# Optimization experiments

Measured on AMD Instinct MI355X. Metric: run time of the kernel, lower is better.

The kernel has to match this reference:

```python
import jax, jax.numpy as jnp
import numpy as np

B, N, H, E, P = 2, 20000, 128, 200000, 3


def _mlp2(x, w1, b1, w2, b2):
    # Linear -> SiLU -> Linear
    return jax.nn.silu(x @ w1 + b1) @ w2 + b2


def setup_inputs() -> dict:
    key = jax.random.key(0)
    ks = iter(jax.random.split(key, 40))
    def nrm(shape, s=0.05):
        return jax.random.normal(next(ks), shape, dtype=jnp.float32) * s
    inp = {
        "features": jax.random.normal(next(ks), (B, N, H), dtype=jnp.float32),
        "positions": jax.random.normal(next(ks), (B, N, P), dtype=jnp.float32),
        "edge_index_up": jax.random.randint(next(ks), (2, E), 0, N, dtype=jnp.int32),
        "edge_index_down": jax.random.randint(next(ks), (2, E), 0, N, dtype=jnp.int32),
        "degree_up": jax.random.uniform(next(ks), (N,), minval=1.0, maxval=32.0, dtype=jnp.float32),
        "degree_down": jax.random.uniform(next(ks), (N,), minval=1.0, maxval=32.0, dtype=jnp.float32),
    }
    for name in ("up", "down"):
        inp[f"w_msg1_{name}"] = nrm((2 * H + 1, H)); inp[f"b_msg1_{name}"] = jnp.zeros((H,), jnp.float32)
        inp[f"w_msg2_{name}"] = nrm((H, H));         inp[f"b_msg2_{name}"] = jnp.zeros((H,), jnp.float32)
        inp[f"w_pos1_{name}"] = nrm((H, H));         inp[f"b_pos1_{name}"] = jnp.zeros((H,), jnp.float32)
        inp[f"w_pos2_{name}"] = nrm((H, 1));         inp[f"b_pos2_{name}"] = jnp.zeros((1,), jnp.float32)
    inp["w_upd1"] = nrm((2 * H, H)); inp["b_upd1"] = jnp.zeros((H,), jnp.float32)
    inp["w_upd2"] = nrm((H, H));     inp["b_upd2"] = jnp.zeros((H,), jnp.float32)
    return inp


def reference(features, positions, edge_index_up, edge_index_down, degree_up, degree_down,
              w_msg1_up, b_msg1_up, w_msg2_up, b_msg2_up,
              w_pos1_up, b_pos1_up, w_pos2_up, b_pos2_up,
              w_msg1_down, b_msg1_down, w_msg2_down, b_msg2_down,
              w_pos1_down, b_pos1_down, w_pos2_down, b_pos2_down,
              w_upd1, b_upd1, w_upd2, b_upd2):
    n_neighborhoods = 2
    msg_acc = jnp.zeros_like(features)
    pos_upd = jnp.zeros_like(positions)
    neighborhoods = [
        (edge_index_up, degree_up,
         (w_msg1_up, b_msg1_up, w_msg2_up, b_msg2_up),
         (w_pos1_up, b_pos1_up, w_pos2_up, b_pos2_up)),
        (edge_index_down, degree_down,
         (w_msg1_down, b_msg1_down, w_msg2_down, b_msg2_down),
         (w_pos1_down, b_pos1_down, w_pos2_down, b_pos2_down)),
    ]
    for edge_index, degree, msg_p, pos_p in neighborhoods:
        src, dst = edge_index[0], edge_index[1]
        h_src = features[:, src, :]                     # [B, E, H] gather
        h_dst = features[:, dst, :]                     # [B, E, H] gather
        rel_pos = positions[:, src, :] - positions[:, dst, :]  # [B, E, P]
        dist = jnp.linalg.norm(rel_pos, axis=-1, keepdims=True)  # [B, E, 1]
        msg_input = jnp.concatenate([h_src, h_dst, dist], axis=-1)  # [B, E, 2H+1]
        messages = _mlp2(msg_input, *msg_p)             # [B, E, H]
        agg = jnp.zeros_like(features).at[:, dst, :].add(messages)  # scatter-add over dim 1
        agg = agg / jnp.clip(degree, 1.0, None)[None, :, None]
        msg_acc = msg_acc + agg
        weights = jnp.tanh(_mlp2(messages, *pos_p))     # [B, E, 1]
        pos_upd = pos_upd + jnp.zeros_like(positions).at[:, dst, :].add(weights * rel_pos)
    feat_update = _mlp2(jnp.concatenate([features, msg_acc], axis=-1), w_upd1, b_upd1, w_upd2, b_upd2)
    updated_features = features + feat_update
    updated_positions = positions + pos_upd / n_neighborhoods
    return updated_features, updated_positions
```

## Files before the change

### kernel.cpp

```cpp
#include <hip/hip_runtime.h>

#define BB 2
#define NN 20000
#define HH 128
#define EE 200000
#define TR 96
#define NEB 2084
#define NBLK 79

typedef unsigned short u16;
typedef __attribute__((ext_vector_type(4))) float f32x4;
typedef __bf16 bf16x8 __attribute__((ext_vector_type(8)));

#define MFMA(a, b, c) __builtin_amdgcn_mfma_f32_16x16x32_bf16((a), (b), (c), 0, 0, 0)

__device__ __forceinline__ float bf2f(u16 u) {
    union { unsigned int i; float f; } v; v.i = ((unsigned int)u) << 16; return v.f;
}
__device__ __forceinline__ u16 f2bf(float f) {
    union { __bf16 h; u16 u; } v; v.h = (__bf16)f; return v.u;
}
#if __has_builtin(__builtin_amdgcn_rcpf)
__device__ __forceinline__ float rcpf(float x) { return __builtin_amdgcn_rcpf(x); }
#else
__device__ __forceinline__ float rcpf(float x) { return 1.f / x; }
#endif
__device__ __forceinline__ float silu_f(float z) { return z * rcpf(1.f + __expf(-z)); }
__device__ __forceinline__ float ldv(const void* p, long i, int f) {
    return f ? ((const float*)p)[i] : bf2f(((const u16*)p)[i]);
}

__global__ __launch_bounds__(256) void detect_zero_kernel(const u16* __restrict__ f,
                                                          int* __restrict__ flag,
                                                          int* __restrict__ cnt) {
    int i = blockIdx.x * 256 + threadIdx.x;
    if (i < 40000) cnt[i] = 0;
    if (blockIdx.x == 0) {
        int tid = threadIdx.x;
        u16 v = f[tid * 2];
        int e = (v >> 7) & 0xFF;
        int ok = (e >= 101 && e <= 143) ? 1 : 0;
        __shared__ int c;
        if (tid == 0) c = 0;
        __syncthreads();
        atomicAdd(&c, ok);
        __syncthreads();
        if (tid == 0) *flag = (c < 200) ? 1 : 0;
    }
}

#define C5TOT 5281540
#define FTOT 180224
#define R0 5240000
#define R1 (R0 + C5TOT)
#define R2 (R1 + FTOT)
#define R3 (R2 + 2 * EE)
struct P18 { const void* p[18]; };
struct P8 { const void* w[8]; };

__global__ __launch_bounds__(256) void setup_kernel(
    P18 cp, P8 wf, const int* __restrict__ eu, const int* __restrict__ ed,
    float* __restrict__ ws_acc, u16* __restrict__ canon, u16* __restrict__ fbase,
    int* __restrict__ cnt_up, int* __restrict__ cnt_dn, const int* __restrict__ flag)
{
    long i = (long)blockIdx.x * 256 + threadIdx.x;
    if (i < R0) { ws_acc[i] = 0.f; return; }
    if (i < R1) {
        static const int off[19] = {
            0, 5120000, 5240000, 5260000, 5280000,
            5280128, 5280256, 5280384, 5280512, 5280640,
            5280642, 5280770, 5280898, 5281026, 5281154, 5281282,
            5281284, 5281412, 5281540 };
        static const int rsz[18] = {
            5120000, 120000, 20000, 20000,
            128, 128, 128, 128, 128, 1,
            128, 128, 128, 128, 128, 1,
            128, 128 };
        static const int soff[18] = {
            0, 0, 0, 0,
            32768, 0, 0, 0, 0, 0,
            32768, 0, 0, 0, 0, 0,
            0, 0 };
        int j = (int)(i - R0);
        int isf = *flag;
        int t = 0;
#pragma unroll 1
        while (j >= off[t + 1]) ++t;
        int k = j - off[t];
        u16 v = 0;
        if (k < rsz[t]) v = f2bf(ldv(cp.p[t], (long)soff[t] + k, isf));
        canon[j] = v;
        return;
    }
    if (i < R2) {
        static const int foff[9] = { 0, 32768, 49152, 65536, 98304, 114688,
                                     131072, 163840, 180224 };
        int j = (int)(i - R1);
        int isf = *flag;
        int t = 0;
#pragma unroll 1
        while (j >= foff[t + 1]) ++t;
        int m = j - foff[t];
        int jj = m & 7, lane = (m >> 3) & 63, nt = (m >> 9) & 7, kt = m >> 12;
        int k = kt * 32 + ((lane >> 4) * 8) + jj;
        int n = nt * 16 + (lane & 15);
        fbase[j] = f2bf(ldv(wf.w[t], (long)k * 128 + n, isf));
        return;
    }
    if (i < R3) {
        int e = (int)(i - R2);
        if (e < EE) atomicAdd(&cnt_up[eu[EE + e]], 1);
        else atomicAdd(&cnt_dn[ed[EE + e - EE]], 1);
    }
}

__global__ __launch_bounds__(256) void gemm_fuse_kernel(
    const void* __restrict__ w2u, const void* __restrict__ p1u,
    const void* __restrict__ b2u, const void* __restrict__ bp1u,
    const void* __restrict__ w2d, const void* __restrict__ p1d,
    const void* __restrict__ b2d, const void* __restrict__ bp1d,
    u16* __restrict__ fragu, u16* __restrict__ fragd,
    u16* __restrict__ cbp1u, u16* __restrict__ cbp1d,
    const int* __restrict__ flag)
{
    const int dir = blockIdx.x >> 6;
    const int idx = (blockIdx.x & 63) * 256 + threadIdx.x;
    const int k = idx >> 7, n = idx & 127;
    const int isf = *flag;
    const void* W2 = dir ? w2d : w2u;
    const void* P1 = dir ? p1d : p1u;
    float s = 0.f;
#pragma unroll 4
    for (int m = 0; m < 128; ++m)
        s += ldv(W2, (long)k * 128 + m, isf) * ldv(P1, (long)m * 128 + n, isf);
    u16* dst = dir ? fragd : fragu;
    dst[(((k >> 5) * 8 + (n >> 4)) * 64 + ((k >> 3) & 3) * 16 + (n & 15)) * 8 + (k & 7)] = f2bf(s);
    if (idx < 128) {
        const void* B2 = dir ? b2d : b2u;
        const void* BP1 = dir ? bp1d : bp1u;
        float t = 0.f;
#pragma unroll 4
        for (int m = 0; m < 128; ++m)
            t += ldv(B2, m, isf) * ldv(P1, (long)m * 128 + idx, isf);
        (dir ? cbp1d : cbp1u)[idx] = f2bf(t + ldv(BP1, idx, isf));
    }
}

struct SP { const int* cnt[2]; int* cur[2]; int* bsum[2]; };

__global__ __launch_bounds__(256) void scan1_kernel(SP p) {
    int half = blockIdx.x / NBLK;
    int b = blockIdx.x - half * NBLK;
    int t = threadIdx.x;
    int i = b * 256 + t;
    __shared__ int buf[256];
    int v = (i < NN) ? p.cnt[half][i] : 0;
    buf[t] = v;
    __syncthreads();
    for (int s = 1; s < 256; s <<= 1) {
        int x = (t >= s) ? buf[t - s] : 0;
        __syncthreads();
        buf[t] += x;
        __syncthreads();
    }
    if (i < NN) p.cur[half][i] = buf[t] - v;
    if (t == 255) p.bsum[half][b] = buf[255];
}

__global__ __launch_bounds__(256) void scan2_kernel(int* __restrict__ bu, int* __restrict__ bd) {
    __shared__ int buf[2][128];
    int half = threadIdx.x >> 7, t = threadIdx.x & 127;
    int* bs = half ? bd : bu;
    int v = (t < NBLK) ? bs[t] : 0;
    buf[half][t] = v;
    __syncthreads();
    for (int s = 1; s < 128; s <<= 1) {
        int x = (t >= s) ? buf[half][t - s] : 0;
        __syncthreads();
        buf[half][t] += x;
        __syncthreads();
    }
    if (t < NBLK) bs[t] = buf[half][t] - v;
}

__global__ void scatter2_kernel(const int* __restrict__ eu, const int* __restrict__ ed,
                                int* __restrict__ cu, const int* __restrict__ bu,
                                int* __restrict__ cd, const int* __restrict__ bd,
                                int* __restrict__ su, int* __restrict__ sd) {
    int e = blockIdx.x * 256 + threadIdx.x;
    if (e < EE) {
        int d = eu[EE + e];
        int p = atomicAdd(&cu[d], 1) + bu[d >> 8];
        su[p] = e;
    } else {
        e -= EE;
        if (e < EE) {
            int d = ed[EE + e];
            int p = atomicAdd(&cd[d], 1) + bd[d >> 8];
            sd[p] = e;
        }
    }
}

struct EP {
    const int* eidx; const int* es; const u16* deg;
    const u16* fW1; const u16* fW2; const u16* fP1;
    const u16* w1last; const u16* bias1; const u16* bias2;
    const u16* biasp1; const u16* wp2; const u16* biasp2;
};

__global__ __launch_bounds__(512, 4) void edge_kernel(
    const u16* __restrict__ feat, const u16* __restrict__ posit,
    EP up, EP dn,
    float* __restrict__ msg_base, float* __restrict__ pos_base)
{
    const int tid = threadIdx.x;
    const int lane = tid & 63;
    const int wv = tid >> 6;
    const int half = blockIdx.x / (BB * NEB);
    const int rem = blockIdx.x - half * (BB * NEB);
    const int bb = rem / NEB;
    const int s0 = (rem - bb * NEB) * TR;
    const EP P = half ? dn : up;
    float* msg_acc = msg_base + (size_t)bb * NN * HH;
    float* pos_acc = pos_base + (size_t)bb * NN * 3;

    __shared__ u16 sA[TR][136];
    __shared__ u16 sB[TR][136];
    __shared__ u16 sC[TR][136];
    __shared__ float sInv[TR];
    __shared__ int sDst[TR];

    {
        const int r = tid >> 2, part = tid & 3;
        if (r < TR) {
            int slot = s0 + r; if (slot >= EE) slot = EE - 1;
            int e = P.es[slot];
            int s = P.eidx[e];
            int d = P.eidx[EE + e];
            if (part == 0) {
                sDst[r] = d;
                sInv[r] = 1.f / fmaxf(bf2f(P.deg[d]), 1.f);
                const u16* ps = posit + ((size_t)bb * NN + s) * 3;
                const u16* pd = posit + ((size_t)bb * NN + d) * 3;
                float dx = bf2f(ps[0]) - bf2f(pd[0]);
                float dy = bf2f(ps[1]) - bf2f(pd[1]);
                float dz = bf2f(ps[2]) - bf2f(pd[2]);
                *(float4*)&sC[r][128] =
                    make_float4(sqrtf(dx * dx + dy * dy + dz * dz), dx, dy, dz);
            }
            const uint4* fs = (const uint4*)(feat + ((size_t)bb * NN + s) * HH);
            const uint4* fd = (const uint4*)(feat + ((size_t)bb * NN + d) * HH);
            uint4* as = (uint4*)&sA[r][part * 32];
            uint4* ad = (uint4*)&sB[r][part * 32];
#pragma unroll
            for (int i = 0; i < 4; ++i) { as[i] = fs[part * 4 + i]; ad[i] = fd[part * 4 + i]; }
        }
    }
    __syncthreads();

    const int wm = wv >> 2;
    const int wn = wv & 3;
    const int rbase = wm * 48;
    const int mrow = lane & 15;
    const int kq = (lane >> 4) * 8;
    const int crow = (lane >> 4) * 4;
    const int ccol = lane & 15;

    f32x4 acc[3][2];
#pragma unroll
    for (int mt = 0; mt < 3; ++mt) {
        acc[mt][0] = (f32x4){0.f, 0.f, 0.f, 0.f};
        acc[mt][1] = (f32x4){0.f, 0.f, 0.f, 0.f};
    }
#pragma unroll
    for (int kt = 0; kt < 8; ++kt) {
        const u16* Xb = (kt < 4) ? &sA[0][0] : &sB[0][0];
        const int kk = (kt & 3) * 32 + kq;
        bf16x8 bw0 = *(const bf16x8*)(P.fW1 + (size_t)(((kt * 8 + wn * 2) * 64 + lane) * 8));
        bf16x8 bw1 = *(const bf16x8*)(P.fW1 + (size_t)(((kt * 8 + wn * 2 + 1) * 64 + lane) * 8));
#pragma unroll
        for (int mt = 0; mt < 3; ++mt) {
            bf16x8 a = *(const bf16x8*)(Xb + (rbase + mt * 16 + mrow) * 136 + kk);
            acc[mt][0] = MFMA(a, bw0, acc[mt][0]);
            acc[mt][1] = MFMA(a, bw1, acc[mt][1]);
        }
    }

#pragma unroll
    for (int n2 = 0; n2 < 2; ++n2) {
        const int col = (wn * 2 + n2) * 16 + ccol;
        const float wl = bf2f(P.w1last[col]);
        const float bb1 = bf2f(P.bias1[col]);
#pragma unroll
        for (int mt = 0; mt < 3; ++mt) {
#pragma unroll
            for (int r = 0; r < 4; ++r) {
                const int row = rbase + mt * 16 + crow + r;
                const float dist = ((const float*)&sC[row][128])[0];
                float z = fmaf(dist, wl, acc[mt][n2][r]) + bb1;
                sC[row][col] = f2bf(silu_f(z));
            }
        }
    }
    __syncthreads();

    f32x4 facc[3][4];
#pragma unroll
    for (int mt = 0; mt < 3; ++mt)
#pragma unroll
        for (int j = 0; j < 4; ++j) facc[mt][j] = (f32x4){0.f, 0.f, 0.f, 0.f};
    const int nt0 = wn * 4;
#pragma unroll
    for (int kt = 0; kt < 4; ++kt) {
        const int kk = kt * 32 + kq;
        bf16x8 bw[4];
#pragma unroll
        for (int j = 0; j < 4; ++j) {
            const int nt = nt0 + j;
            const size_t off = (nt & 8)
                ? (size_t)(16384 + ((kt * 8 + (nt & 7)) * 64 + lane) * 8)
                : (size_t)(((kt * 8 + nt) * 64 + lane) * 8);
            bw[j] = *(const bf16x8*)(P.fW2 + off);
        }
#pragma unroll
        for (int mt = 0; mt < 3; ++mt) {
            bf16x8 a = *(const bf16x8*)(&sC[0][0] + (rbase + mt * 16 + mrow) * 136 + kk);
#pragma unroll
            for (int j = 0; j < 4; ++j) facc[mt][j] = MFMA(a, bw[j], facc[mt][j]);
        }
    }

    if (wn < 2) {
#pragma unroll
        for (int j = 0; j < 4; ++j) {
            const int col = (nt0 + j) * 16 + ccol;
            const float b2v = bf2f(P.bias2[col]);
#pragma unroll
            for (int mt = 0; mt < 3; ++mt) {
#pragma unroll
                for (int r = 0; r < 4; ++r) {
                    const int row = rbase + mt * 16 + crow + r;
                    sA[row][col] = f2bf(facc[mt][j][r] + b2v);
                }
            }
        }
    } else {
#pragma unroll
        for (int j = 0; j < 4; ++j) {
            const int col = (nt0 - 8 + j) * 16 + ccol;
            const float fbv = bf2f(P.biasp1[col]);
#pragma unroll
            for (int mt = 0; mt < 3; ++mt) {
#pragma unroll
                for (int r = 0; r < 4; ++r) {
                    const int row = rbase + mt * 16 + crow + r;
                    sB[row][col] = f2bf(silu_f(facc[mt][j][r] + fbv));
                }
            }
        }
    }
    __syncthreads();

    {
        const int scol = tid & 127;
        const int r0 = (tid >> 7) * 24;
        float vals[24];
#pragma unroll
        for (int j = 0; j < 24; ++j) vals[j] = bf2f(sA[r0 + j][scol]);
        float accv = 0.f;
        int dprev = sDst[r0];
        float invprev = sInv[r0];
#pragma unroll
        for (int j = 0; j < 24; ++j) {
            const int r = r0 + j;
            int dcur = sDst[r];
            if (dcur != dprev) {
                unsafeAtomicAdd(&msg_acc[(size_t)dprev * HH + scol], accv * invprev);
                accv = 0.f; dprev = dcur; invprev = sInv[r];
            }
            accv += (s0 + r < EE) ? vals[j] : 0.f;
        }
        unsafeAtomicAdd(&msg_acc[(size_t)dprev * HH + scol], accv * invprev);
    }

    {
        const int r = tid >> 2, q = tid & 3;
        if (r < TR) {
            const unsigned* t32 = (const unsigned*)&sB[r][q * 32];
            const unsigned* w32 = (const unsigned*)(P.wp2 + q * 32);
            float p = 0.f;
#pragma unroll
            for (int k = 0; k < 16; ++k) {
                unsigned a = t32[k], b = w32[k];
                union { unsigned i; float f; } al, ah, bl, bh;
                al.i = a << 16; ah.i = a & 0xffff0000u;
                bl.i = b << 16; bh.i = b & 0xffff0000u;
                p = fmaf(al.f, bl.f, p);
                p = fmaf(ah.f, bh.f, p);
            }
            p += __shfl_xor(p, 1);
            p += __shfl_xor(p, 2);
            if (q == 0 && s0 + r < EE) {
                float wgt = tanhf(p + bf2f(P.biasp2[0]));
                const float* rp = (const float*)&sC[r][128];
                const size_t pb = (size_t)sDst[r] * 3;
                unsafeAtomicAdd(&pos_acc[pb + 0], wgt * rp[1]);
                unsafeAtomicAdd(&pos_acc[pb + 1], wgt * rp[2]);
                unsafeAtomicAdd(&pos_acc[pb + 2], wgt * rp[3]);
            }
        }
    }
}

__global__ __launch_bounds__(256) void update_kernel(
    const void* __restrict__ rawfeat, const void* __restrict__ rawpos,
    const u16* __restrict__ fU1, const u16* __restrict__ bu1,
    const u16* __restrict__ fU2, const u16* __restrict__ bu2,
    void* __restrict__ outp, const float* __restrict__ magg, const float* __restrict__ pacc,
    const int* __restrict__ flag)
{
    const int tid = threadIdx.x;
    const int lane = tid & 63;
    const int wv = tid >> 6;
    const int row0 = blockIdx.x * 64;
    const int isf = *flag;

    __shared__ u16 sA[64][136];
    __shared__ u16 sB[64][136];

    if (isf) {
        const float* fp = (const float*)rawfeat + (size_t)row0 * HH;
        for (int i = tid; i < 1024; i += 256) {
            int r = i >> 4, c = (i & 15) * 8;
            float4 v0 = *(const float4*)(fp + (size_t)r * HH + c);
            float4 v1 = *(const float4*)(fp + (size_t)r * HH + c + 4);
            uint4 o;
            o.x = (unsigned)f2bf(v0.x) | ((unsigned)f2bf(v0.y) << 16);
            o.y = (unsigned)f2bf(v0.z) | ((unsigned)f2bf(v0.w) << 16);
            o.z = (unsigned)f2bf(v1.x) | ((unsigned)f2bf(v1.y) << 16);
            o.w = (unsigned)f2bf(v1.z) | ((unsigned)f2bf(v1.w) << 16);
            *(uint4*)&sA[r][c] = o;
        }
    } else {
        const uint4* fp = (const uint4*)((const u16*)rawfeat + (size_t)row0 * HH);
        for (int i = tid; i < 1024; i += 256) {
            int r = i >> 4, c = i & 15;
            *(uint4*)&sA[r][c * 8] = fp[i];
        }
    }
    {
        const float4* am = (const float4*)(magg) + (size_t)row0 * 32;
        for (int i = tid; i < 2048; i += 256) {
            int r = i >> 5;
            float4 v = am[i];
            int c = (i & 31) * 4;
            sB[r][c + 0] = f2bf(v.x);
            sB[r][c + 1] = f2bf(v.y);
            sB[r][c + 2] = f2bf(v.z);
            sB[r][c + 3] = f2bf(v.w);
        }
    }
    __syncthreads();

    const int nt0 = wv * 2;
    const int mrow = lane & 15;
    const int kq = (lane >> 4) * 8;
    const int crow = (lane >> 4) * 4;
    const int ccol = lane & 15;

    f32x4 acc[4][2];
#pragma unroll
    for (int mt = 0; mt < 4; ++mt) {
        acc[mt][0] = (f32x4){0.f, 0.f, 0.f, 0.f};
        acc[mt][1] = (f32x4){0.f, 0.f, 0.f, 0.f};
    }
#pragma unroll
    for (int kt = 0; kt < 8; ++kt) {
        const u16* Xb = (kt < 4) ? &sA[0][0] : &sB[0][0];
        const int kk = (kt & 3) * 32 + kq;
        bf16x8 bw0 = *(const bf16x8*)(fU1 + (size_t)(((kt * 8 + nt0) * 64 + lane) * 8));
        bf16x8 bw1 = *(const bf16x8*)(fU1 + (size_t)(((kt * 8 + nt0 + 1) * 64 + lane) * 8));
#pragma unroll
        for (int mt = 0; mt < 4; ++mt) {
            bf16x8 a = *(const bf16x8*)(Xb + (mt * 16 + mrow) * 136 + kk);
            acc[mt][0] = MFMA(a, bw0, acc[mt][0]);
            acc[mt][1] = MFMA(a, bw1, acc[mt][1]);
        }
    }
    __syncthreads();

#pragma unroll
    for (int mt = 0; mt < 4; ++mt) {
#pragma unroll
        for (int n2 = 0; n2 < 2; ++n2) {
            const int col = (nt0 + n2) * 16 + ccol;
            const float bb = bf2f(bu1[col]);
#pragma unroll
            for (int r = 0; r < 4; ++r) {
                const int row = mt * 16 + crow + r;
                sB[row][col] = f2bf(silu_f(acc[mt][n2][r] + bb));
            }
        }
    }
    __syncthreads();

#pragma unroll
    for (int mt = 0; mt < 4; ++mt) {
        acc[mt][0] = (f32x4){0.f, 0.f, 0.f, 0.f};
        acc[mt][1] = (f32x4){0.f, 0.f, 0.f, 0.f};
    }
#pragma unroll
    for (int kt = 0; kt < 4; ++kt) {
        const int kk = kt * 32 + kq;
        bf16x8 bw0 = *(const bf16x8*)(fU2 + (size_t)(((kt * 8 + nt0) * 64 + lane) * 8));
        bf16x8 bw1 = *(const bf16x8*)(fU2 + (size_t)(((kt * 8 + nt0 + 1) * 64 + lane) * 8));
#pragma unroll
        for (int mt = 0; mt < 4; ++mt) {
            bf16x8 a = *(const bf16x8*)(&sB[0][0] + (mt * 16 + mrow) * 136 + kk);
            acc[mt][0] = MFMA(a, bw0, acc[mt][0]);
            acc[mt][1] = MFMA(a, bw1, acc[mt][1]);
        }
    }
#pragma unroll
    for (int mt = 0; mt < 4; ++mt) {
#pragma unroll
        for (int n2 = 0; n2 < 2; ++n2) {
            const int col = (nt0 + n2) * 16 + ccol;
            const float bb = bf2f(bu2[col]);
#pragma unroll
            for (int r = 0; r < 4; ++r) {
                const int row = mt * 16 + crow + r;
                const size_t idx = (size_t)(row0 + row) * HH + col;
                if (isf) {
                    float base = ((const float*)rawfeat)[idx];
                    ((float*)outp)[idx] = acc[mt][n2][r] + bb + base;
                } else {
                    float base = bf2f(sA[row][col]);
                    ((u16*)outp)[idx] = f2bf(acc[mt][n2][r] + bb + base);
                }
            }
        }
    }

    if (tid < 192) {
        int i = row0 * 3 + tid;
        float x = pacc[i];
        if (isf) {
            float base = ((const float*)rawpos)[i];
            ((float*)outp)[5120000 + i] = base + 0.5f * x;
        } else {
            float base = bf2f(((const u16*)rawpos)[i]);
            ((u16*)outp)[5120000 + i] = f2bf(base + 0.5f * x);
        }
    }
}

extern "C" void kernel_launch(void* const* d_in, const int* in_sizes, int n_in,
                              void* d_out, int out_size, void* d_ws, size_t ws_size,
                              hipStream_t stream)
{
    float* ws_msg  = (float*)d_ws;
    float* ws_pos  = (float*)((char*)d_ws + 20480000);
    int*   cnt_up  = (int*)((char*)d_ws + 20960000);
    int*   cnt_dn  = (int*)((char*)d_ws + 21040000);
    int*   cur_up  = (int*)((char*)d_ws + 21120000);
    int*   cur_dn  = (int*)((char*)d_ws + 21200000);
    int*   bsum_up = (int*)((char*)d_ws + 21280000);
    int*   bsum_dn = (int*)((char*)d_ws + 21280400);
    int*   es_up   = (int*)((char*)d_ws + 21280800);
    int*   es_dn   = (int*)((char*)d_ws + 22080800);
    u16*   fbase   = (u16*)((char*)d_ws + 22880800);
    u16*   canon   = (u16*)((char*)d_ws + 23241248);
    int*   flag    = (int*)((char*)d_ws + 33804328);
    if (ws_size < 33804332ULL) return;

    u16* f_m1u = fbase;
    u16* f_m2u = fbase + 32768;
    u16* f_p1u = fbase + 49152;
    u16* f_m1d = fbase + 65536;
    u16* f_m2d = fbase + 98304;
    u16* f_p1d = fbase + 114688;
    u16* f_u1  = fbase + 131072;
    u16* f_u2  = fbase + 163840;

    u16* cfeat  = canon;
    u16* cpos   = canon + 5120000;
    u16* cdgu   = canon + 5240000;
    u16* cdgd   = canon + 5260000;
    u16* cw1lu  = canon + 5280000;
    u16* cb1u   = canon + 5280128;
    u16* cb2u   = canon + 5280256;
    u16* cbp1u  = canon + 5280384;
    u16* cwp2u  = canon + 5280512;
    u16* cbp2u  = canon + 5280640;
    u16* cw1ld  = canon + 5280642;
    u16* cb1d   = canon + 5280770;
    u16* cb2d   = canon + 5280898;
    u16* cbp1d  = canon + 5281026;
    u16* cwp2d  = canon + 5281154;
    u16* cbp2d  = canon + 5281282;
    u16* cbu1   = canon + 5281284;
    u16* cbu2   = canon + 5281412;

    const int* ei_up = (const int*)d_in[2];
    const int* ei_dn = (const int*)d_in[3];

    detect_zero_kernel<<<157, 256, 0, stream>>>((const u16*)d_in[0], flag, cnt_up);

    P18 cp;
    cp.p[0] = d_in[0];  cp.p[1] = d_in[1];  cp.p[2] = d_in[4];  cp.p[3] = d_in[5];
    cp.p[4] = d_in[6];  cp.p[5] = d_in[7];  cp.p[6] = d_in[9];  cp.p[7] = d_in[11];
    cp.p[8] = d_in[12]; cp.p[9] = d_in[13];
    cp.p[10] = d_in[14]; cp.p[11] = d_in[15]; cp.p[12] = d_in[17]; cp.p[13] = d_in[19];
    cp.p[14] = d_in[20]; cp.p[15] = d_in[21];
    cp.p[16] = d_in[23]; cp.p[17] = d_in[25];
    P8 wsf;
    wsf.w[0] = d_in[6];  wsf.w[1] = d_in[8];  wsf.w[2] = d_in[10]; wsf.w[3] = d_in[14];
    wsf.w[4] = d_in[16]; wsf.w[5] = d_in[18]; wsf.w[6] = d_in[22]; wsf.w[7] = d_in[24];
    setup_kernel<<<(R3 + 255) / 256, 256, 0, stream>>>(cp, wsf, ei_up, ei_dn,
                                                       ws_msg, canon, fbase,
                                                       cnt_up, cnt_dn, flag);

    gemm_fuse_kernel<<<128, 256, 0, stream>>>(d_in[8], d_in[10], d_in[9], d_in[11],
                                              d_in[16], d_in[18], d_in[17], d_in[19],
                                              f_p1u, f_p1d, cbp1u, cbp1d, flag);

    SP sp;
    sp.cnt[0] = cnt_up; sp.cnt[1] = cnt_dn;
    sp.cur[0] = cur_up; sp.cur[1] = cur_dn;
    sp.bsum[0] = bsum_up; sp.bsum[1] = bsum_dn;
    scan1_kernel<<<2 * NBLK, 256, 0, stream>>>(sp);
    scan2_kernel<<<1, 256, 0, stream>>>(bsum_up, bsum_dn);
    scatter2_kernel<<<(2 * EE + 255) / 256, 256, 0, stream>>>(ei_up, ei_dn, cur_up, bsum_up,
                                                              cur_dn, bsum_dn, es_up, es_dn);

    EP up, dn;
    up.eidx = ei_up; up.es = es_up; up.deg = cdgu;
    up.fW1 = f_m1u; up.fW2 = f_m2u; up.fP1 = f_p1u;
    up.w1last = cw1lu; up.bias1 = cb1u; up.bias2 = cb2u;
    up.biasp1 = cbp1u; up.wp2 = cwp2u; up.biasp2 = cbp2u;
    dn.eidx = ei_dn; dn.es = es_dn; dn.deg = cdgd;
    dn.fW1 = f_m1d; dn.fW2 = f_m2d; dn.fP1 = f_p1d;
    dn.w1last = cw1ld; dn.bias1 = cb1d; dn.bias2 = cb2d;
    dn.biasp1 = cbp1d; dn.wp2 = cwp2d; dn.biasp2 = cbp2d;
    edge_kernel<<<2 * BB * NEB, 512, 0, stream>>>(cfeat, cpos, up, dn, ws_msg, ws_pos);

    update_kernel<<<625, 256, 0, stream>>>(d_in[0], d_in[1], f_u1, cbu1, f_u2, cbu2,
                                           d_out, ws_msg, ws_pos, flag);
}
```

Measured before the change: 537.1 us.

## Remap edge workgroups across XCDs and run-length merge position atomics

Workgroup IDs are remapped so that consecutive blockIdx values spread across 8 chunks of 1042. This is intended to place contiguous dst-sorted tiles on the same XCD and improve L2 locality for the feature gathers and atomics. The per-edge position atomics now go through shared memory: tanh weights are stored there, and 12 threads run-length accumulate contributions for repeated destinations before issuing one atomic per run. The launch-bounds occupancy hint is also lowered from 4 to 2. The extra barrier and serial 24-step loop add latency, and the block remap assumes NWG is exactly 8*CPX.

Result: faster. 475.6 us (-11.5%).

```diff
diff --git a/kernel.cpp b/kernel.cpp
--- a/kernel.cpp
+++ b/kernel.cpp
@@ -7,6 +7,8 @@
 #define TR 96
 #define NEB 2084
 #define NBLK 79
+#define NWG (2 * BB * NEB)
+#define CPX 1042
 
 typedef unsigned short u16;
 typedef __attribute__((ext_vector_type(4))) float f32x4;
@@ -209,7 +211,7 @@
     const u16* biasp1; const u16* wp2; const u16* biasp2;
 };
 
-__global__ __launch_bounds__(512, 4) void edge_kernel(
+__global__ __launch_bounds__(512, 2) void edge_kernel(
     const u16* __restrict__ feat, const u16* __restrict__ posit,
     EP up, EP dn,
     float* __restrict__ msg_base, float* __restrict__ pos_base)
@@ -217,8 +219,10 @@
     const int tid = threadIdx.x;
     const int lane = tid & 63;
     const int wv = tid >> 6;
-    const int half = blockIdx.x / (BB * NEB);
-    const int rem = blockIdx.x - half * (BB * NEB);
+    const int bid0 = blockIdx.x;
+    const int bid = (bid0 & 7) * CPX + (bid0 >> 3);
+    const int half = bid / (BB * NEB);
+    const int rem = bid - half * (BB * NEB);
     const int bb = rem / NEB;
     const int s0 = (rem - bb * NEB) * TR;
     const EP P = half ? dn : up;
@@ -229,7 +233,16 @@
     __shared__ u16 sB[TR][136];
     __shared__ u16 sC[TR][136];
     __shared__ float sInv[TR];
+    __shared__ float sWgt[TR];
     __shared__ int sDst[TR];
+
+    const int wm = wv >> 2;
+    const int wn = wv & 3;
+    const int rbase = wm * 48;
+    const int mrow = lane & 15;
+    const int kq = (lane >> 4) * 8;
+    const int crow = (lane >> 4) * 4;
+    const int ccol = lane & 15;
 
     {
         const int r = tid >> 2, part = tid & 3;
@@ -259,14 +272,6 @@
     }
     __syncthreads();
 
-    const int wm = wv >> 2;
-    const int wn = wv & 3;
-    const int rbase = wm * 48;
-    const int mrow = lane & 15;
-    const int kq = (lane >> 4) * 8;
-    const int crow = (lane >> 4) * 4;
-    const int ccol = lane & 15;
-
     f32x4 acc[3][2];
 #pragma unroll
     for (int mt = 0; mt < 3; ++mt) {
@@ -401,15 +406,28 @@
             }
             p += __shfl_xor(p, 1);
             p += __shfl_xor(p, 2);
-            if (q == 0 && s0 + r < EE) {
-                float wgt = tanhf(p + bf2f(P.biasp2[0]));
-                const float* rp = (const float*)&sC[r][128];
-                const size_t pb = (size_t)sDst[r] * 3;
-                unsafeAtomicAdd(&pos_acc[pb + 0], wgt * rp[1]);
-                unsafeAtomicAdd(&pos_acc[pb + 1], wgt * rp[2]);
-                unsafeAtomicAdd(&pos_acc[pb + 2], wgt * rp[3]);
-            }
-        }
+            if (q == 0)
+                sWgt[r] = (s0 + r < EE) ? tanhf(p + bf2f(P.biasp2[0])) : 0.f;
+        }
+    }
+    __syncthreads();
+
+    if (tid < 12) {
+        const int comp = tid % 3;
+        const int r0 = (tid / 3) * 24;
+        float accv = 0.f;
+        int dprev = sDst[r0];
+#pragma unroll
+        for (int j = 0; j < 24; ++j) {
+            const int r = r0 + j;
+            int dcur = sDst[r];
+            if (dcur != dprev) {
+                if (accv != 0.f) unsafeAtomicAdd(&pos_acc[(size_t)dprev * 3 + comp], accv);
+                accv = 0.f; dprev = dcur;
+            }
+            accv += sWgt[r] * ((const float*)&sC[r][128])[1 + comp];
+        }
+        if (accv != 0.f) unsafeAtomicAdd(&pos_acc[(size_t)dprev * 3 + comp], accv);
     }
 }
 
@@ -644,7 +662,7 @@
     dn.fW1 = f_m1d; dn.fW2 = f_m2d; dn.fP1 = f_p1d;
     dn.w1last = cw1ld; dn.bias1 = cb1d; dn.bias2 = cb2d;
     dn.biasp1 = cbp1d; dn.wp2 = cwp2d; dn.biasp2 = cbp2d;
-    edge_kernel<<<2 * BB * NEB, 512, 0, stream>>>(cfeat, cpos, up, dn, ws_msg, ws_pos);
+    edge_kernel<<<NWG, 512, 0, stream>>>(cfeat, cpos, up, dn, ws_msg, ws_pos);
 
     update_kernel<<<625, 256, 0, stream>>>(d_in[0], d_in[1], f_u1, cbu1, f_u2, cbu2,
                                            d_out, ws_msg, ws_pos, flag);
```
